# Optimization experiments

Hardware: AMD Instinct MI355X
Metric: run time of the kernel (lower is better)

The kernel has to match this reference:

```python
import jax, jax.numpy as jnp
import numpy as np

B, T, C, H = 4, 2048, 1024, 64


def setup_inputs() -> dict:
    key = jax.random.key(0)
    kx, kk, kq, kv = jax.random.split(key, 4)
    scale = 1.0 / np.sqrt(C)
    return {
        "x": jax.random.normal(kx, (B, T, C), dtype=jnp.float32),
        "Wk": jax.random.normal(kk, (C, H), dtype=jnp.float32) * scale,
        "Wq": jax.random.normal(kq, (C, H), dtype=jnp.float32) * scale,
        "Wv": jax.random.normal(kv, (C, H), dtype=jnp.float32) * scale,
    }


def reference(x, Wk, Wq, Wv):
    # projections: [B, T, H]
    k = jnp.einsum("btc,ch->bth", x, Wk)
    q = jnp.einsum("btc,ch->bth", x, Wq)
    v = jnp.einsum("btc,ch->bth", x, Wv)
    # attention scores [B, T, T], scaled by sqrt(head_size)
    scores = jnp.einsum("bqh,bkh->bqk", q, k) / jnp.sqrt(jnp.asarray(H, x.dtype))
    # causal mask (decoder)
    causal = jnp.tril(jnp.ones((T, T), dtype=bool))
    scores = jnp.where(causal, scores, -jnp.inf)
    attn = jax.nn.softmax(scores, axis=-1)
    # dropout p=0.0 (eval) -> identity
    return jnp.einsum("bqk,bkh->bqh", attn, v)
```

## Files before the change

kernel.cpp:

```cpp
#include <hip/hip_runtime.h>
#include <hip/hip_bf16.h>

#define BB 4
#define TT 2048
#define CC 1024
#define HH 64
#define LOG2E 1.4426950408889634f
#define QSCALE (0.125f * LOG2E)

typedef __attribute__((ext_vector_type(8))) unsigned short ushort8;
typedef __attribute__((ext_vector_type(4))) unsigned short ushort4v;
typedef __attribute__((ext_vector_type(8))) __bf16 bf16x8;
typedef __attribute__((ext_vector_type(4))) float float4v;

static __device__ __forceinline__ unsigned short f2bf(float f) {
    return __builtin_bit_cast(unsigned short, (__bf16)f);
}

static __device__ __forceinline__ float4v mfma16(ushort8 a, ushort8 b, float4v c) {
    return __builtin_amdgcn_mfma_f32_16x16x32_bf16(
        __builtin_bit_cast(bf16x8, a), __builtin_bit_cast(bf16x8, b), c, 0, 0, 0);
}

static __device__ __forceinline__ ushort8 cvt8(float4v a, float4v b) {
    ushort8 r;
#pragma unroll
    for (int i = 0; i < 4; ++i) { r[i] = f2bf(a[i]); r[4 + i] = f2bf(b[i]); }
    return r;
}

#define BARRIER()                                            \
    do {                                                     \
        asm volatile("s_waitcnt lgkmcnt(0)" ::: "memory");   \
        __builtin_amdgcn_s_barrier();                        \
        asm volatile("" ::: "memory");                       \
    } while (0)

__global__ __launch_bounds__(256) void wconv_kernel(
    const float* __restrict__ Wq, const float* __restrict__ Wk,
    const float* __restrict__ Wv, unsigned short* __restrict__ wf)
{
    __shared__ __align__(16) float wsT[3][64][68];
    const int kc = blockIdx.x / 6, part = blockIdx.x % 6;
    const int t = threadIdx.x;
    const int r = t >> 2, c0 = (t & 3) << 4;
    const float* Ws[3] = {Wq, Wk, Wv};
#pragma unroll
    for (int y = 0; y < 3; ++y) {
        const float* src = Ws[y] + (size_t)(kc * 64 + r) * HH + c0;
        const float sc = (y == 0) ? QSCALE : 1.0f;
#pragma unroll
        for (int i = 0; i < 16; ++i) wsT[y][c0 + i][r] = src[i] * sc;
    }
    __syncthreads();
    const int U = part * 256 + t;
    const int lane = U & 63, qq = U >> 6;
    const int nt = qq % 12, ks = qq / 12;
    const int y = nt >> 2;
    const int col = 16 * (nt & 3) + (lane & 15);
    const int kl = ks * 32 + 8 * (lane >> 4);
    float4v v0 = *(const float4v*)&wsT[y][col][kl];
    float4v v1 = *(const float4v*)&wsT[y][col][kl + 4];
    *(ushort8*)&wf[((size_t)kc * 1536 + U) * 8] = cvt8(v0, v1);
}

__global__ __launch_bounds__(384) void proj_kernel(
    const float* __restrict__ x, const unsigned short* __restrict__ wf,
    unsigned short* __restrict__ qo, unsigned short* __restrict__ ko,
    unsigned short* __restrict__ vo)
{
    __shared__ __align__(16) unsigned short xa[2][1024];

    const int t0 = blockIdx.x << 4;
    const int tid = threadIdx.x;
    const int w = tid >> 6;
    const int lane = tid & 63;
    const int l15 = lane & 15, g = lane >> 4;
    const int nt0 = 2 * w;

    const bool stg = tid < 128;
    const int sr = tid >> 3, su = tid & 7;
    const int soff = (sr * 8 + (su ^ (sr & 7))) * 8;
    const float* xp = x + (size_t)(t0 + sr) * CC + su * 8;

    float4v xr[4][2];
    if (stg) {
#pragma unroll
        for (int p = 0; p < 4; ++p) {
            xr[p][0] = *(const float4v*)(xp + p * 64);
            xr[p][1] = *(const float4v*)(xp + p * 64 + 4);
        }
    }

    const unsigned short* wp = wf + ((size_t)nt0 * 64 + lane) * 8;
    ushort8 bc[2][2], bn[2][2];
#pragma unroll
    for (int ks = 0; ks < 2; ++ks)
#pragma unroll
        for (int j = 0; j < 2; ++j) {
            bc[j][ks] = *(const ushort8*)(wp + (size_t)ks * 6144 + j * 512);
            bn[j][ks] = *(const ushort8*)(wp + (size_t)(2 + ks) * 6144 + j * 512);
        }

    if (stg) *(ushort8*)&xa[0][soff] = cvt8(xr[0][0], xr[0][1]);
    BARRIER();

    const int sw = l15 & 7;
    const int r00 = (l15 * 8 + (g ^ sw)) * 8;
    const int r01 = (l15 * 8 + ((4 + g) ^ sw)) * 8;

    float4v acc[2];
    acc[0] = (float4v)0.0f; acc[1] = (float4v)0.0f;

#pragma unroll
    for (int kc = 0; kc < 16; ++kc) {
        const int cur = kc & 1;
        if (stg && kc + 4 < 16) {
            xr[kc & 3][0] = *(const float4v*)(xp + (kc + 4) * 64);
            xr[kc & 3][1] = *(const float4v*)(xp + (kc + 4) * 64 + 4);
        }
        ushort8 nw[2][2];
        if (kc + 2 < 16) {
#pragma unroll
            for (int ks = 0; ks < 2; ++ks)
#pragma unroll
                for (int j = 0; j < 2; ++j)
                    nw[j][ks] = *(const ushort8*)
                        (wp + (size_t)(2 * kc + 4 + ks) * 6144 + j * 512);
        }
        ushort8 a0 = *(const ushort8*)&xa[cur][r00];
        ushort8 a1 = *(const ushort8*)&xa[cur][r01];
        if (w < 4) {
#pragma unroll
            for (int j = 0; j < 2; ++j) {
                acc[j] = mfma16(a0, bc[j][0], acc[j]);
                acc[j] = mfma16(a1, bc[j][1], acc[j]);
            }
        } else {
#pragma unroll
            for (int j = 0; j < 2; ++j) {
                acc[j] = mfma16(bc[j][0], a0, acc[j]);
                acc[j] = mfma16(bc[j][1], a1, acc[j]);
            }
        }
        if (stg && kc + 1 < 16)
            *(ushort8*)&xa[cur ^ 1][soff] =
                cvt8(xr[(kc + 1) & 3][0], xr[(kc + 1) & 3][1]);
        BARRIER();
#pragma unroll
        for (int ks = 0; ks < 2; ++ks)
#pragma unroll
            for (int j = 0; j < 2; ++j) {
                bc[j][ks] = bn[j][ks];
                if (kc + 2 < 16) bn[j][ks] = nw[j][ks];
            }
    }

    if (w < 4) {
        unsigned short* dst = (w < 2) ? qo : ko;
#pragma unroll
        for (int j = 0; j < 2; ++j) {
            const int nf = (nt0 + j) & 3;
#pragma unroll
            for (int r = 0; r < 4; ++r)
                dst[(size_t)(t0 + 4 * g + r) * HH + 16 * nf + l15] =
                    f2bf(acc[j][r]);
        }
    } else {
        const int b = t0 >> 11, tl = t0 & (TT - 1);
#pragma unroll
        for (int j = 0; j < 2; ++j) {
            const int nf = nt0 + j - 8;
#pragma unroll
            for (int r = 0; r < 4; ++r)
                vo[((size_t)b * HH + 16 * nf + 4 * g + r) * TT + tl + l15] =
                    f2bf(acc[j][r]);
        }
    }
}

__global__ __launch_bounds__(512, 2) void attn_kernel(
    const unsigned short* __restrict__ qw,
    const unsigned short* __restrict__ kw,
    const unsigned short* __restrict__ vw,
    float* __restrict__ out)
{
    __shared__ float om[8][16];
    __shared__ float olg[8][4][16];
    __shared__ __align__(16) float oo[8][16][64];

    const int idx = blockIdx.x;
    const int b = idx & (BB - 1);
    const int j = idx >> 2;
    const int tid = threadIdx.x;
    const int w = tid >> 6;
    const int lane = tid & 63;
    const int l15 = lane & 15;
    const int g = lane >> 4;

    const unsigned short* kb = kw + (size_t)b * TT * HH;
    const unsigned short* vb = vw + (size_t)b * HH * TT;

    for (int ph = 0; ph < 2; ++ph) {
        const int qt = ph ? j : (TT / 16 - 1) - j;
        const int q0 = qt << 4;
        const int q = q0 + l15;

        const unsigned short* qrow = qw + (size_t)(b * TT + q) * HH + 8 * g;
        ushort8 qf0 = *(const ushort8*)qrow;
        ushort8 qf1 = *(const ushort8*)(qrow + 32);

        float m_run = -3.0e38f, l_run = 0.0f;
        float4v o[4];
#pragma unroll
        for (int i = 0; i < 4; ++i) o[i] = (float4v)0.0f;

        for (int kv0 = 64 * w; kv0 < q0 + 16; kv0 += 512) {
            const unsigned short* kr = kb + (size_t)(kv0 + l15) * HH + 8 * g;
            ushort8 akl[4], akh[4];
#pragma unroll
            for (int f = 0; f < 4; ++f) {
                akl[f] = *(const ushort8*)(kr + f * 16 * HH);
                akh[f] = *(const ushort8*)(kr + f * 16 * HH + 32);
            }
            ushort8 av[4][2];
#pragma unroll
            for (int ht = 0; ht < 4; ++ht) {
                const unsigned short* vp =
                    vb + (size_t)(16 * ht + l15) * TT + kv0 + 4 * g;
#pragma unroll
                for (int g2 = 0; g2 < 2; ++g2) {
                    ushort4v v0 = *(const ushort4v*)(vp + 32 * g2);
                    ushort4v v1 = *(const ushort4v*)(vp + 32 * g2 + 16);
#pragma unroll
                    for (int r = 0; r < 4; ++r) {
                        av[ht][g2][r] = v0[r];
                        av[ht][g2][4 + r] = v1[r];
                    }
                }
            }

            float4v s[4];
#pragma unroll
            for (int f = 0; f < 4; ++f) {
                s[f] = mfma16(akl[f], qf0, (float4v)0.0f);
                s[f] = mfma16(akh[f], qf1, s[f]);
            }

            if (kv0 + 63 > q0) {
#pragma unroll
                for (int f = 0; f < 4; ++f)
#pragma unroll
                    for (int r = 0; r < 4; ++r)
                        if (kv0 + 16 * f + 4 * g + r > q) s[f][r] = -1e30f;
            }

            float mt = s[0][0];
#pragma unroll
            for (int f = 0; f < 4; ++f)
#pragma unroll
                for (int r = 0; r < 4; ++r) mt = fmaxf(mt, s[f][r]);
            mt = fmaxf(mt, __shfl_xor(mt, 16, 64));
            mt = fmaxf(mt, __shfl_xor(mt, 32, 64));

            const float m_new = fmaxf(m_run, mt);
            const float scale = exp2f(m_run - m_new);
            float sum = 0.0f;
#pragma unroll
            for (int f = 0; f < 4; ++f)
#pragma unroll
                for (int r = 0; r < 4; ++r) {
                    s[f][r] = exp2f(s[f][r] - m_new);
                    sum += s[f][r];
                }
            l_run = l_run * scale + sum;
            m_run = m_new;
#pragma unroll
            for (int i = 0; i < 4; ++i) o[i] *= scale;

            ushort8 bp[2];
#pragma unroll
            for (int r = 0; r < 4; ++r) {
                bp[0][r] = f2bf(s[0][r]); bp[0][4 + r] = f2bf(s[1][r]);
                bp[1][r] = f2bf(s[2][r]); bp[1][4 + r] = f2bf(s[3][r]);
            }
#pragma unroll
            for (int ht = 0; ht < 4; ++ht) {
                o[ht] = mfma16(av[ht][0], bp[0], o[ht]);
                o[ht] = mfma16(av[ht][1], bp[1], o[ht]);
            }
        }

        if (lane < 16) om[w][lane] = m_run;
        olg[w][g][l15] = l_run;
#pragma unroll
        for (int ht = 0; ht < 4; ++ht)
            *(float4v*)&oo[w][l15][16 * ht + 4 * g] = o[ht];
        __syncthreads();

#pragma unroll 2
        for (int e = tid; e < 16 * HH; e += 512) {
            const int qq = e >> 6, h = e & 63;
            float mstar = om[0][qq];
#pragma unroll
            for (int w2 = 1; w2 < 8; ++w2) mstar = fmaxf(mstar, om[w2][qq]);
            float lsum = 0.0f, osum = 0.0f;
#pragma unroll
            for (int w2 = 0; w2 < 8; ++w2) {
                const float al = exp2f(om[w2][qq] - mstar);
                const float lw = olg[w2][0][qq] + olg[w2][1][qq] +
                                 olg[w2][2][qq] + olg[w2][3][qq];
                lsum += al * lw;
                osum += al * oo[w2][qq][h];
            }
            out[((size_t)b * TT + q0 + qq) * HH + h] = osum / lsum;
        }
        __syncthreads();
    }
}

extern "C" void kernel_launch(void* const* d_in, const int* in_sizes, int n_in,
                              void* d_out, int out_size, void* d_ws, size_t ws_size,
                              hipStream_t stream) {
    const float* x  = (const float*)d_in[0];
    const float* Wk = (const float*)d_in[1];
    const float* Wq = (const float*)d_in[2];
    const float* Wv = (const float*)d_in[3];

    unsigned short* q_ws  = (unsigned short*)d_ws;
    unsigned short* k_ws  = q_ws + (size_t)BB * TT * HH;
    unsigned short* vt_ws = k_ws + (size_t)BB * TT * HH;
    unsigned short* wf_ws = vt_ws + (size_t)BB * TT * HH;

    wconv_kernel<<<96, 256, 0, stream>>>(Wq, Wk, Wv, wf_ws);
    proj_kernel<<<BB * TT / 16, 384, 0, stream>>>(x, wf_ws, q_ws, k_ws, vt_ws);
    attn_kernel<<<BB * TT / 32, 512, 0, stream>>>(q_ws, k_ws, vt_ws, (float*)d_out);
}
```

Baseline: 50.33 us.

## Retile projection to 64 rows and split attention into partial and merge kernels

The projection kernel now handles 64 tokens per block with 8 waves, each computing a 32x48 tile so more weight-fragment reuse comes from each load. Attention is restructured from a per-block 8-wave KV split with in-block merge into a split-KV partial kernel: 320 blocks each cover a 64-query tile over one KV segment of up to 512 keys, with K fragments prefetched one step ahead. A separate merge kernel combines the segments' max, sum and output partials. This balances the causal triangle across blocks, at the cost of an extra launch and a round trip of fp32 partials through global memory.

```diff
diff --git a/kernel.cpp b/kernel.cpp
--- a/kernel.cpp
+++ b/kernel.cpp
@@ -64,258 +64,303 @@
     *(ushort8*)&wf[((size_t)kc * 1536 + U) * 8] = cvt8(v0, v1);
 }
 
-__global__ __launch_bounds__(384) void proj_kernel(
+__global__ __launch_bounds__(512, 2) void proj_kernel(
     const float* __restrict__ x, const unsigned short* __restrict__ wf,
     unsigned short* __restrict__ qo, unsigned short* __restrict__ ko,
     unsigned short* __restrict__ vo)
 {
-    __shared__ __align__(16) unsigned short xa[2][1024];
-
-    const int t0 = blockIdx.x << 4;
+    __shared__ __align__(16) unsigned short xa[2][4096];
+
+    const int t0 = blockIdx.x << 6;
     const int tid = threadIdx.x;
     const int w = tid >> 6;
     const int lane = tid & 63;
     const int l15 = lane & 15, g = lane >> 4;
-    const int nt0 = 2 * w;
-
-    const bool stg = tid < 128;
+    const int mh = w & 1, ng = w >> 1;
+    const int nt0 = 3 * ng;
+
     const int sr = tid >> 3, su = tid & 7;
     const int soff = (sr * 8 + (su ^ (sr & 7))) * 8;
     const float* xp = x + (size_t)(t0 + sr) * CC + su * 8;
 
     float4v xr[4][2];
-    if (stg) {
-#pragma unroll
-        for (int p = 0; p < 4; ++p) {
-            xr[p][0] = *(const float4v*)(xp + p * 64);
-            xr[p][1] = *(const float4v*)(xp + p * 64 + 4);
-        }
-    }
-
-    const unsigned short* wp = wf + ((size_t)nt0 * 64 + lane) * 8;
-    ushort8 bc[2][2], bn[2][2];
-#pragma unroll
-    for (int ks = 0; ks < 2; ++ks)
-#pragma unroll
-        for (int j = 0; j < 2; ++j) {
-            bc[j][ks] = *(const ushort8*)(wp + (size_t)ks * 6144 + j * 512);
-            bn[j][ks] = *(const ushort8*)(wp + (size_t)(2 + ks) * 6144 + j * 512);
-        }
-
-    if (stg) *(ushort8*)&xa[0][soff] = cvt8(xr[0][0], xr[0][1]);
+#pragma unroll
+    for (int p = 0; p < 4; ++p) {
+        xr[p][0] = *(const float4v*)(xp + p * 64);
+        xr[p][1] = *(const float4v*)(xp + p * 64 + 4);
+    }
+
+    const unsigned short* wpj[3];
+#pragma unroll
+    for (int jj = 0; jj < 3; ++jj)
+        wpj[jj] = wf + ((size_t)(nt0 + jj) * 64 + lane) * 8;
+    ushort8 bc[3][2], bn[3][2];
+#pragma unroll
+    for (int jj = 0; jj < 3; ++jj)
+#pragma unroll
+        for (int ks = 0; ks < 2; ++ks) {
+            bc[jj][ks] = *(const ushort8*)(wpj[jj] + (size_t)ks * 6144);
+            bn[jj][ks] = *(const ushort8*)(wpj[jj] + (size_t)(2 + ks) * 6144);
+        }
+
+    *(ushort8*)&xa[0][soff] = cvt8(xr[0][0], xr[0][1]);
     BARRIER();
 
-    const int sw = l15 & 7;
-    const int r00 = (l15 * 8 + (g ^ sw)) * 8;
-    const int r01 = (l15 * 8 + ((4 + g) ^ sw)) * 8;
-
-    float4v acc[2];
-    acc[0] = (float4v)0.0f; acc[1] = (float4v)0.0f;
-
+    const int row0 = 32 * mh + l15, row1 = row0 + 16;
+    const int a00 = (row0 * 8 + (g ^ (row0 & 7))) * 8;
+    const int a01 = (row0 * 8 + ((4 + g) ^ (row0 & 7))) * 8;
+    const int a10 = (row1 * 8 + (g ^ (row1 & 7))) * 8;
+    const int a11 = (row1 * 8 + ((4 + g) ^ (row1 & 7))) * 8;
+
+    float4v acc[2][3];
+#pragma unroll
+    for (int mt = 0; mt < 2; ++mt)
+#pragma unroll
+        for (int jj = 0; jj < 3; ++jj) acc[mt][jj] = (float4v)0.0f;
+
+    const bool isv = nt0 + 2 >= 8 && nt0 >= 8;
 #pragma unroll
     for (int kc = 0; kc < 16; ++kc) {
         const int cur = kc & 1;
-        if (stg && kc + 4 < 16) {
+        if (kc + 4 < 16) {
             xr[kc & 3][0] = *(const float4v*)(xp + (kc + 4) * 64);
             xr[kc & 3][1] = *(const float4v*)(xp + (kc + 4) * 64 + 4);
         }
-        ushort8 nw[2][2];
+        ushort8 nw[3][2];
         if (kc + 2 < 16) {
 #pragma unroll
-            for (int ks = 0; ks < 2; ++ks)
-#pragma unroll
-                for (int j = 0; j < 2; ++j)
-                    nw[j][ks] = *(const ushort8*)
-                        (wp + (size_t)(2 * kc + 4 + ks) * 6144 + j * 512);
-        }
-        ushort8 a0 = *(const ushort8*)&xa[cur][r00];
-        ushort8 a1 = *(const ushort8*)&xa[cur][r01];
-        if (w < 4) {
-#pragma unroll
-            for (int j = 0; j < 2; ++j) {
-                acc[j] = mfma16(a0, bc[j][0], acc[j]);
-                acc[j] = mfma16(a1, bc[j][1], acc[j]);
-            }
-        } else {
-#pragma unroll
-            for (int j = 0; j < 2; ++j) {
-                acc[j] = mfma16(bc[j][0], a0, acc[j]);
-                acc[j] = mfma16(bc[j][1], a1, acc[j]);
-            }
-        }
-        if (stg && kc + 1 < 16)
+            for (int jj = 0; jj < 3; ++jj)
+#pragma unroll
+                for (int ks = 0; ks < 2; ++ks)
+                    nw[jj][ks] = *(const ushort8*)
+                        (wpj[jj] + (size_t)(2 * kc + 4 + ks) * 6144);
+        }
+        ushort8 af00 = *(const ushort8*)&xa[cur][a00];
+        ushort8 af01 = *(const ushort8*)&xa[cur][a01];
+        ushort8 af10 = *(const ushort8*)&xa[cur][a10];
+        ushort8 af11 = *(const ushort8*)&xa[cur][a11];
+#pragma unroll
+        for (int jj = 0; jj < 3; ++jj) {
+            if (nt0 + jj < 8) {
+                acc[0][jj] = mfma16(af00, bc[jj][0], acc[0][jj]);
+                acc[0][jj] = mfma16(af01, bc[jj][1], acc[0][jj]);
+                acc[1][jj] = mfma16(af10, bc[jj][0], acc[1][jj]);
+                acc[1][jj] = mfma16(af11, bc[jj][1], acc[1][jj]);
+            } else {
+                acc[0][jj] = mfma16(bc[jj][0], af00, acc[0][jj]);
+                acc[0][jj] = mfma16(bc[jj][1], af01, acc[0][jj]);
+                acc[1][jj] = mfma16(bc[jj][0], af10, acc[1][jj]);
+                acc[1][jj] = mfma16(bc[jj][1], af11, acc[1][jj]);
+            }
+        }
+        if (kc + 1 < 16)
             *(ushort8*)&xa[cur ^ 1][soff] =
                 cvt8(xr[(kc + 1) & 3][0], xr[(kc + 1) & 3][1]);
         BARRIER();
 #pragma unroll
-        for (int ks = 0; ks < 2; ++ks)
-#pragma unroll
-            for (int j = 0; j < 2; ++j) {
-                bc[j][ks] = bn[j][ks];
-                if (kc + 2 < 16) bn[j][ks] = nw[j][ks];
-            }
-    }
-
-    if (w < 4) {
-        unsigned short* dst = (w < 2) ? qo : ko;
-#pragma unroll
-        for (int j = 0; j < 2; ++j) {
-            const int nf = (nt0 + j) & 3;
-#pragma unroll
-            for (int r = 0; r < 4; ++r)
-                dst[(size_t)(t0 + 4 * g + r) * HH + 16 * nf + l15] =
-                    f2bf(acc[j][r]);
-        }
-    } else {
-        const int b = t0 >> 11, tl = t0 & (TT - 1);
-#pragma unroll
-        for (int j = 0; j < 2; ++j) {
-            const int nf = nt0 + j - 8;
-#pragma unroll
-            for (int r = 0; r < 4; ++r)
-                vo[((size_t)b * HH + 16 * nf + 4 * g + r) * TT + tl + l15] =
-                    f2bf(acc[j][r]);
-        }
-    }
-}
-
-__global__ __launch_bounds__(512, 2) void attn_kernel(
+        for (int jj = 0; jj < 3; ++jj)
+#pragma unroll
+            for (int ks = 0; ks < 2; ++ks) {
+                bc[jj][ks] = bn[jj][ks];
+                if (kc + 2 < 16) bn[jj][ks] = nw[jj][ks];
+            }
+    }
+    (void)isv;
+
+    const int bb = t0 >> 11, tloc = t0 & (TT - 1);
+#pragma unroll
+    for (int jj = 0; jj < 3; ++jj) {
+        const int nt = nt0 + jj;
+#pragma unroll
+        for (int mt = 0; mt < 2; ++mt) {
+            float4v a = acc[mt][jj];
+            if (nt < 4) {
+#pragma unroll
+                for (int r = 0; r < 4; ++r)
+                    qo[(size_t)(t0 + 32 * mh + 16 * mt + 4 * g + r) * HH +
+                       16 * nt + l15] = f2bf(a[r]);
+            } else if (nt < 8) {
+#pragma unroll
+                for (int r = 0; r < 4; ++r)
+                    ko[(size_t)(t0 + 32 * mh + 16 * mt + 4 * g + r) * HH +
+                       16 * (nt - 4) + l15] = f2bf(a[r]);
+            } else {
+#pragma unroll
+                for (int r = 0; r < 4; ++r)
+                    vo[((size_t)bb * HH + 16 * (nt - 8) + 4 * g + r) * TT +
+                       tloc + 32 * mh + 16 * mt + l15] = f2bf(a[r]);
+            }
+        }
+    }
+}
+
+__global__ __launch_bounds__(256, 2) void attn_partial_kernel(
     const unsigned short* __restrict__ qw,
     const unsigned short* __restrict__ kw,
     const unsigned short* __restrict__ vw,
-    float* __restrict__ out)
+    float* __restrict__ om_ws, float* __restrict__ ol_ws,
+    float* __restrict__ oo_ws)
 {
-    __shared__ float om[8][16];
-    __shared__ float olg[8][4][16];
-    __shared__ __align__(16) float oo[8][16][64];
-
-    const int idx = blockIdx.x;
-    const int b = idx & (BB - 1);
-    const int j = idx >> 2;
+    const int s = blockIdx.x;
+    const int b = s & 3;
+    const int t = 79 - (s >> 2);
+    int j, seg;
+    if (t < 8)       { j = t;                   seg = 0; }
+    else if (t < 24) { j = 8 + ((t - 8) >> 1);  seg = (t - 8) & 1; }
+    else if (t < 48) { j = 16 + (t - 24) / 3;   seg = (t - 24) % 3; }
+    else             { j = 24 + ((t - 48) >> 2); seg = (t - 48) & 3; }
+
     const int tid = threadIdx.x;
     const int w = tid >> 6;
     const int lane = tid & 63;
-    const int l15 = lane & 15;
-    const int g = lane >> 4;
+    const int l15 = lane & 15, g = lane >> 4;
+    const int q0w = 64 * j + 16 * w;
+    const int q = q0w + l15;
+
+    const unsigned short* qrow = qw + (size_t)(b * TT + q) * HH + 8 * g;
+    ushort8 qf0 = *(const ushort8*)qrow;
+    ushort8 qf1 = *(const ushort8*)(qrow + 32);
 
     const unsigned short* kb = kw + (size_t)b * TT * HH;
     const unsigned short* vb = vw + (size_t)b * HH * TT;
 
-    for (int ph = 0; ph < 2; ++ph) {
-        const int qt = ph ? j : (TT / 16 - 1) - j;
-        const int q0 = qt << 4;
-        const int q = q0 + l15;
-
-        const unsigned short* qrow = qw + (size_t)(b * TT + q) * HH + 8 * g;
-        ushort8 qf0 = *(const ushort8*)qrow;
-        ushort8 qf1 = *(const ushort8*)(qrow + 32);
-
-        float m_run = -3.0e38f, l_run = 0.0f;
-        float4v o[4];
-#pragma unroll
-        for (int i = 0; i < 4; ++i) o[i] = (float4v)0.0f;
-
-        for (int kv0 = 64 * w; kv0 < q0 + 16; kv0 += 512) {
-            const unsigned short* kr = kb + (size_t)(kv0 + l15) * HH + 8 * g;
-            ushort8 akl[4], akh[4];
+    const int kstart = 512 * seg;
+    const int kend = min(kstart + 512, 64 * j + 64);
+    const int kend_w = min(kend, q0w + 16);
+
+    float m_run = -3.0e38f, l_run = 0.0f;
+    float4v o[4];
+#pragma unroll
+    for (int i = 0; i < 4; ++i) o[i] = (float4v)0.0f;
+
+    ushort8 kl[4], kh[4];
+    {
+        const unsigned short* kr = kb + (size_t)(kstart + l15) * HH + 8 * g;
+#pragma unroll
+        for (int f = 0; f < 4; ++f) {
+            kl[f] = *(const ushort8*)(kr + f * 16 * HH);
+            kh[f] = *(const ushort8*)(kr + f * 16 * HH + 32);
+        }
+    }
+
+    for (int kv0 = kstart; kv0 < kend_w; kv0 += 64) {
+        ushort8 av[4][2];
+#pragma unroll
+        for (int ht = 0; ht < 4; ++ht) {
+            const unsigned short* vp =
+                vb + (size_t)(16 * ht + l15) * TT + kv0 + 4 * g;
+#pragma unroll
+            for (int g2 = 0; g2 < 2; ++g2) {
+                ushort4v v0 = *(const ushort4v*)(vp + 32 * g2);
+                ushort4v v1 = *(const ushort4v*)(vp + 32 * g2 + 16);
+#pragma unroll
+                for (int r = 0; r < 4; ++r) {
+                    av[ht][g2][r] = v0[r];
+                    av[ht][g2][4 + r] = v1[r];
+                }
+            }
+        }
+        ushort8 nkl[4], nkh[4];
+        const bool more = kv0 + 64 < kend_w;
+        if (more) {
+            const unsigned short* kr = kb + (size_t)(kv0 + 64 + l15) * HH + 8 * g;
 #pragma unroll
             for (int f = 0; f < 4; ++f) {
-                akl[f] = *(const ushort8*)(kr + f * 16 * HH);
-                akh[f] = *(const ushort8*)(kr + f * 16 * HH + 32);
-            }
-            ushort8 av[4][2];
-#pragma unroll
-            for (int ht = 0; ht < 4; ++ht) {
-                const unsigned short* vp =
-                    vb + (size_t)(16 * ht + l15) * TT + kv0 + 4 * g;
-#pragma unroll
-                for (int g2 = 0; g2 < 2; ++g2) {
-                    ushort4v v0 = *(const ushort4v*)(vp + 32 * g2);
-                    ushort4v v1 = *(const ushort4v*)(vp + 32 * g2 + 16);
-#pragma unroll
-                    for (int r = 0; r < 4; ++r) {
-                        av[ht][g2][r] = v0[r];
-                        av[ht][g2][4 + r] = v1[r];
-                    }
-                }
-            }
-
-            float4v s[4];
-#pragma unroll
-            for (int f = 0; f < 4; ++f) {
-                s[f] = mfma16(akl[f], qf0, (float4v)0.0f);
-                s[f] = mfma16(akh[f], qf1, s[f]);
-            }
-
-            if (kv0 + 63 > q0) {
-#pragma unroll
-                for (int f = 0; f < 4; ++f)
-#pragma unroll
-                    for (int r = 0; r < 4; ++r)
-                        if (kv0 + 16 * f + 4 * g + r > q) s[f][r] = -1e30f;
-            }
-
-            float mt = s[0][0];
+                nkl[f] = *(const ushort8*)(kr + f * 16 * HH);
+                nkh[f] = *(const ushort8*)(kr + f * 16 * HH + 32);
+            }
+        }
+
+        float4v sc[4];
+#pragma unroll
+        for (int f = 0; f < 4; ++f) {
+            sc[f] = mfma16(kl[f], qf0, (float4v)0.0f);
+            sc[f] = mfma16(kh[f], qf1, sc[f]);
+        }
+
+        if (kv0 + 63 > q0w) {
 #pragma unroll
             for (int f = 0; f < 4; ++f)
 #pragma unroll
-                for (int r = 0; r < 4; ++r) mt = fmaxf(mt, s[f][r]);
-            mt = fmaxf(mt, __shfl_xor(mt, 16, 64));
-            mt = fmaxf(mt, __shfl_xor(mt, 32, 64));
-
-            const float m_new = fmaxf(m_run, mt);
-            const float scale = exp2f(m_run - m_new);
-            float sum = 0.0f;
-#pragma unroll
-            for (int f = 0; f < 4; ++f)
-#pragma unroll
-                for (int r = 0; r < 4; ++r) {
-                    s[f][r] = exp2f(s[f][r] - m_new);
-                    sum += s[f][r];
-                }
-            l_run = l_run * scale + sum;
-            m_run = m_new;
-#pragma unroll
-            for (int i = 0; i < 4; ++i) o[i] *= scale;
-
-            ushort8 bp[2];
+                for (int r = 0; r < 4; ++r)
+                    if (kv0 + 16 * f + 4 * g + r > q) sc[f][r] = -1e30f;
+        }
+
+        float mt = sc[0][0];
+#pragma unroll
+        for (int f = 0; f < 4; ++f)
+#pragma unroll
+            for (int r = 0; r < 4; ++r) mt = fmaxf(mt, sc[f][r]);
+        mt = fmaxf(mt, __shfl_xor(mt, 16, 64));
+        mt = fmaxf(mt, __shfl_xor(mt, 32, 64));
+
+        const float m_new = fmaxf(m_run, mt);
+        const float scale = exp2f(m_run - m_new);
+        float sum = 0.0f;
+#pragma unroll
+        for (int f = 0; f < 4; ++f)
 #pragma unroll
             for (int r = 0; r < 4; ++r) {
-                bp[0][r] = f2bf(s[0][r]); bp[0][4 + r] = f2bf(s[1][r]);
-                bp[1][r] = f2bf(s[2][r]); bp[1][4 + r] = f2bf(s[3][r]);
-            }
-#pragma unroll
-            for (int ht = 0; ht < 4; ++ht) {
-                o[ht] = mfma16(av[ht][0], bp[0], o[ht]);
-                o[ht] = mfma16(av[ht][1], bp[1], o[ht]);
-            }
-        }
-
-        if (lane < 16) om[w][lane] = m_run;
-        olg[w][g][l15] = l_run;
-#pragma unroll
-        for (int ht = 0; ht < 4; ++ht)
-            *(float4v*)&oo[w][l15][16 * ht + 4 * g] = o[ht];
-        __syncthreads();
-
-#pragma unroll 2
-        for (int e = tid; e < 16 * HH; e += 512) {
-            const int qq = e >> 6, h = e & 63;
-            float mstar = om[0][qq];
-#pragma unroll
-            for (int w2 = 1; w2 < 8; ++w2) mstar = fmaxf(mstar, om[w2][qq]);
-            float lsum = 0.0f, osum = 0.0f;
-#pragma unroll
-            for (int w2 = 0; w2 < 8; ++w2) {
-                const float al = exp2f(om[w2][qq] - mstar);
-                const float lw = olg[w2][0][qq] + olg[w2][1][qq] +
-                                 olg[w2][2][qq] + olg[w2][3][qq];
-                lsum += al * lw;
-                osum += al * oo[w2][qq][h];
-            }
-            out[((size_t)b * TT + q0 + qq) * HH + h] = osum / lsum;
-        }
-        __syncthreads();
+                sc[f][r] = exp2f(sc[f][r] - m_new);
+                sum += sc[f][r];
+            }
+        l_run = l_run * scale + sum;
+        m_run = m_new;
+#pragma unroll
+        for (int i = 0; i < 4; ++i) o[i] *= scale;
+
+        ushort8 bp[2];
+#pragma unroll
+        for (int r = 0; r < 4; ++r) {
+            bp[0][r] = f2bf(sc[0][r]); bp[0][4 + r] = f2bf(sc[1][r]);
+            bp[1][r] = f2bf(sc[2][r]); bp[1][4 + r] = f2bf(sc[3][r]);
+        }
+#pragma unroll
+        for (int ht = 0; ht < 4; ++ht) {
+            o[ht] = mfma16(av[ht][0], bp[0], o[ht]);
+            o[ht] = mfma16(av[ht][1], bp[1], o[ht]);
+        }
+        if (more) {
+#pragma unroll
+            for (int f = 0; f < 4; ++f) { kl[f] = nkl[f]; kh[f] = nkh[f]; }
+        }
+    }
+
+    l_run += __shfl_xor(l_run, 16, 64);
+    l_run += __shfl_xor(l_run, 32, 64);
+
+    const size_t p = (size_t)(b * 32 + j) * 4 + seg;
+    if (lane < 16) {
+        om_ws[p * 64 + 16 * w + l15] = m_run;
+        ol_ws[p * 64 + 16 * w + l15] = l_run;
+    }
+#pragma unroll
+    for (int ht = 0; ht < 4; ++ht)
+        *(float4v*)&oo_ws[(p * 64 + 16 * w + l15) * 64 + 16 * ht + 4 * g] = o[ht];
+}
+
+__global__ __launch_bounds__(256) void attn_merge_kernel(
+    const float* __restrict__ om_ws, const float* __restrict__ ol_ws,
+    const float* __restrict__ oo_ws, float* __restrict__ out)
+{
+    const int b = blockIdx.x & 3, j = blockIdx.x >> 2;
+    const int nseg = (j >> 3) + 1;
+    const size_t base = (size_t)(b * 32 + j) * 4;
+    const int tid = threadIdx.x;
+#pragma unroll 4
+    for (int k = 0; k < 16; ++k) {
+        const int e = tid + 256 * k;
+        const int row = e >> 6, h = e & 63;
+        float mstar = -3.0e38f;
+        for (int p2 = 0; p2 < nseg; ++p2)
+            mstar = fmaxf(mstar, om_ws[(base + p2) * 64 + row]);
+        float lsum = 0.0f, osum = 0.0f;
+        for (int p2 = 0; p2 < nseg; ++p2) {
+            const float al = exp2f(om_ws[(base + p2) * 64 + row] - mstar);
+            lsum += al * ol_ws[(base + p2) * 64 + row];
+            osum += al * oo_ws[((base + p2) * 64 + row) * 64 + h];
+        }
+        out[((size_t)b * TT + 64 * j + row) * HH + h] = osum / lsum;
     }
 }
 
@@ -331,8 +376,14 @@
     unsigned short* k_ws  = q_ws + (size_t)BB * TT * HH;
     unsigned short* vt_ws = k_ws + (size_t)BB * TT * HH;
     unsigned short* wf_ws = vt_ws + (size_t)BB * TT * HH;
+    float* om_ws = (float*)(wf_ws + 196608);
+    float* ol_ws = om_ws + 512 * 64;
+    float* oo_ws = ol_ws + 512 * 64;
 
     wconv_kernel<<<96, 256, 0, stream>>>(Wq, Wk, Wv, wf_ws);
-    proj_kernel<<<BB * TT / 16, 384, 0, stream>>>(x, wf_ws, q_ws, k_ws, vt_ws);
-    attn_kernel<<<BB * TT / 32, 512, 0, stream>>>(q_ws, k_ws, vt_ws, (float*)d_out);
-}
+    proj_kernel<<<BB * TT / 64, 512, 0, stream>>>(x, wf_ws, q_ws, k_ws, vt_ws);
+    attn_partial_kernel<<<320, 256, 0, stream>>>(q_ws, k_ws, vt_ws,
+                                                 om_ws, ol_ws, oo_ws);
+    attn_merge_kernel<<<128, 256, 0, stream>>>(om_ws, ol_ws, oo_ws,
+                                               (float*)d_out);
+}
```

Measured after the change: 94.05 us. 1.87x slower.
